# Performance work log

Measured on AMD Instinct MI355X. Metric: run time of the kernel, lower is better.

The kernel has to match this reference:

```python
import jax, jax.numpy as jnp
import numpy as np

NUM_HEADS = 16
EPS = 1e-5

def _lif(z, vth=1.0):
    # MyNode with fresh membrane and a single call: out = (0/tau + z >= vth)
    return (z >= vth).astype(z.dtype)

def _bn(z, g, b):
    # BatchNorm1d in train mode on (M, C, N): batch stats over (M, N)
    mu = z.mean(axis=(0, 2), keepdims=True)
    var = ((z - mu) ** 2).mean(axis=(0, 2), keepdims=True)
    return g[None, :, None] * (z - mu) * jax.lax.rsqrt(var + EPS) + b[None, :, None]

def _conv1(z, w, bias=None):
    # 1x1 Conv1d: (M, C, N) x (D, C) -> (M, D, N)
    out = jnp.einsum('mcn,dc->mdn', z, w)
    if bias is not None:
        out = out + bias[None, :, None]
    return out

def _rpb_matrix(P, N):
    # vectorized SCA_VA.compute_RPB_matrix: B[i*W+j, k*W+l] = P[(i-k)+M-1, (j-l)+M-1]
    Hs = int(round(N ** 0.5)); M = Hs + 1
    d = jnp.arange(Hs)[:, None] - jnp.arange(Hs)[None, :] + (M - 1)  # (Hs, Hs)
    Bm = P[d[:, None, :, None], d[None, :, None, :]]  # [i, j, k, l]
    return Bm.reshape(N, N)

def _sca(x, y, W, G, Bt, rpb=None):
    # shared body of SCA_AV / SCA_VA; W:(4,C,C) = [q,k,v,proj], G/Bt:(4,C) BN affine
    T, B, C, N = x.shape
    H = NUM_HEADS; D = C // H
    xf = x.reshape(T * B, C, N); yf = y.reshape(T * B, C, N)
    def branch(src, i):
        s = _lif(_bn(_conv1(src, W[i]), G[i], Bt[i]))  # (TB, C, N) binary spikes
        return s.reshape(T, B, C, N).transpose(0, 1, 3, 2).reshape(T, B, N, H, D).transpose(0, 1, 3, 2, 4)
    q = branch(xf, 0)  # (T,B,H,N,D)
    k = branch(yf, 1)
    v = branch(yf, 2)
    attn = jnp.einsum('tbhnd,tbhmd->tbhnm', q, k)  # no softmax: raw spike q@k^T
    if rpb is not None:
        attn = _lif(attn + rpb[None, None, None])  # rpb_lif (v_threshold=1.0)
    o = jnp.einsum('tbhnm,tbhmd->tbhnd', attn, v) * 0.25  # self.scale = 0.25
    o = o.transpose(0, 1, 2, 4, 3).reshape(T, B, C, N)
    o = _lif(o.reshape(T * B, C, N), 0.5)  # attn_lif v_threshold=0.5
    o = _lif(_bn(_conv1(o, W[3]), G[3], Bt[3]))  # proj_conv + proj_bn + proj_lif
    return o.reshape(T, B, C, N)

def _forward(x, y, av_w, av_g, av_b, va_w, va_g, va_b, P_rpb,
             fc1_w, fc1_b, fc2_w, fc2_b,
             m1_w, m1_b, m1_g, m1_bb, m2_w, m2_b, m2_g, m2_bb):
    T, B, C, N = x.shape
    # cross-modal spiking attention (visual->audio and audio->visual)
    x1 = x + _sca(x, y, av_w, av_g, av_b)                       # SCA_AV(x, y)
    y1 = y + _sca(y, x, va_w, va_g, va_b, rpb=_rpb_matrix(P_rpb, N))  # SCA_VA(y, x)
    # CMCI fusion: Linear on channel dim of transposed tensors, then LIF
    zx = jnp.einsum('tbcn,dc->tbdn', x1, fc1_w) + fc1_b[None, None, :, None]
    zy = jnp.einsum('tbcn,dc->tbdn', y1, fc2_w) + fc2_b[None, None, :, None]
    cur = _lif(zx + zy)  # (T,B,C,N)
    # MLPBlock: residual MLP (conv1x1 -> BN -> LIF) x 2
    cf = cur.reshape(T * B, C, N)
    h = _lif(_bn(_conv1(cf, m1_w, m1_b), m1_g, m1_bb))
    o = _lif(_bn(_conv1(h, m2_w, m2_b), m2_g, m2_bb))
    return cur + o.reshape(T, B, C, N)

def setup_inputs() -> dict:
    key = jax.random.key(0)
    ks = jax.random.split(key, 16)
    T, B, C, N = 4, 8, 256, 196
    Hd = 4 * C
    M2 = 2 * (int(N ** 0.5) + 1) - 1  # 29
    s = 0.05
    return {
        'x': jax.random.normal(ks[0], (T, B, C, N), jnp.float32),
        'y': jax.random.normal(ks[1], (T, B, C, N), jnp.float32),
        'av_w': jax.random.normal(ks[2], (4, C, C), jnp.float32) * s,
        'av_g': jnp.ones((4, C), jnp.float32),
        'av_b': jnp.zeros((4, C), jnp.float32),
        'va_w': jax.random.normal(ks[3], (4, C, C), jnp.float32) * s,
        'va_g': jnp.ones((4, C), jnp.float32),
        'va_b': jnp.zeros((4, C), jnp.float32),
        'P_rpb': jax.random.normal(ks[4], (M2, M2), jnp.float32),
        'fc1_w': jax.random.normal(ks[5], (C, C), jnp.float32) * s,
        'fc1_b': jnp.zeros((C,), jnp.float32),
        'fc2_w': jax.random.normal(ks[6], (C, C), jnp.float32) * s,
        'fc2_b': jnp.zeros((C,), jnp.float32),
        'm1_w': jax.random.normal(ks[7], (Hd, C), jnp.float32) * s,
        'm1_b': jnp.zeros((Hd,), jnp.float32),
        'm1_g': jnp.ones((Hd,), jnp.float32),
        'm1_bb': jnp.zeros((Hd,), jnp.float32),
        'm2_w': jax.random.normal(ks[8], (C, Hd), jnp.float32) * s,
        'm2_b': jnp.zeros((C,), jnp.float32),
        'm2_g': jnp.ones((C,), jnp.float32),
        'm2_bb': jnp.zeros((C,), jnp.float32),
    }

def reference(x, y, av_w, av_g, av_b, va_w, va_g, va_b, P_rpb,
              fc1_w, fc1_b, fc2_w, fc2_b,
              m1_w, m1_b, m1_g, m1_bb, m2_w, m2_b, m2_g, m2_bb):
    return _forward(x, y, av_w, av_g, av_b, va_w, va_g, va_b, P_rpb,
                    fc1_w, fc1_b, fc2_w, fc2_b,
                    m1_w, m1_b, m1_g, m1_bb, m2_w, m2_b, m2_g, m2_bb)
```

## Files before the change

### kernel.cpp

```cpp
#include <hip/hip_runtime.h>
#include <math.h>

#define TBB 32
#define CC  256
#define NN  196
#define NJ  (TBB * NN)
#define HD  1024
#define SLAB   ((size_t)TBB * CC * NN)
#define SLAB1K ((size_t)TBB * HD * NN)

struct Ptr6  { const float* p[6]; };
struct PtrM6 { float*       p[6]; };

struct GArg {
    const float* W;  const float* In;
    const float* W2; const float* In2;
    const float* bias; const float* bias2;
    float* Z;
};
struct GArgs { GArg a[6]; };

__device__ __forceinline__ void async_copy16(const float* gsrc, float* ldst)
{
    typedef __attribute__((address_space(1))) void GV;
    typedef __attribute__((address_space(3))) void LV;
    __builtin_amdgcn_global_load_lds((GV*)const_cast<float*>(gsrc), (LV*)ldst,
                                     16, 0, 0);
}

__global__ __launch_bounds__(256) void gemm2(GArgs ga, int Cout, int Cin, int mode)
{
    __shared__ __align__(16) float As[2][16][68];
    __shared__ __align__(16) float Bs[2][16][64];

    const GArg g = ga.a[blockIdx.z];
    const int t  = threadIdx.x;
    const int tx = t & 15, ty = t >> 4;
    const int d0 = blockIdx.x * 64;
    const int j0 = blockIdx.y * 64;
    const int lane = t & 63, wave = t >> 6;

    const int wrow = t >> 2;
    const int wk   = (t & 3) * 4;

    const int brow = wave * 4 + (lane >> 4);
    const int bj   = j0 + (lane & 15) * 4;
    const int bm   = bj / NN;
    const int bn   = bj - bm * NN;
    const size_t bbase = (size_t)bm * Cin * NN + bn;
    float* bdst0 = &Bs[0][wave * 4][0];
    float* bdst1 = &Bs[1][wave * 4][0];

    float acc[4][4] = {{0.f}};
    float4 wreg;

    for (int pass = 0; pass < 2; ++pass) {
        const float* Wp = pass ? g.W2 : g.W;
        const float* Ip = pass ? g.In2 : g.In;
        if (Wp == nullptr) break;
        const int nkt = Cin >> 4;
        const size_t wbase = (size_t)(d0 + wrow) * Cin + wk;

        async_copy16(Ip + bbase + (size_t)brow * NN, bdst0);
        wreg = *(const float4*)(Wp + wbase);
        As[0][wk + 0][wrow] = wreg.x;
        As[0][wk + 1][wrow] = wreg.y;
        As[0][wk + 2][wrow] = wreg.z;
        As[0][wk + 3][wrow] = wreg.w;
        __syncthreads();

        for (int kt = 0; kt < nkt; ++kt) {
            const int  cur  = kt & 1;
            const int  nxt  = cur ^ 1;
            const bool more = (kt + 1) < nkt;
            if (more) {
                const int k0n = (kt + 1) << 4;
                async_copy16(Ip + bbase + (size_t)(k0n + brow) * NN,
                             nxt ? bdst1 : bdst0);
                wreg = *(const float4*)(Wp + wbase + k0n);
            }
            #pragma unroll
            for (int kk = 0; kk < 16; ++kk) {
                const float4 a4 = *(const float4*)(&As[cur][kk][ty * 4]);
                const float4 b4 = *(const float4*)(&Bs[cur][kk][tx * 4]);
                const float ar[4] = {a4.x, a4.y, a4.z, a4.w};
                const float br[4] = {b4.x, b4.y, b4.z, b4.w};
                #pragma unroll
                for (int i = 0; i < 4; ++i)
                    #pragma unroll
                    for (int jj = 0; jj < 4; ++jj)
                        acc[i][jj] = fmaf(ar[i], br[jj], acc[i][jj]);
            }
            if (more) {
                As[nxt][wk + 0][wrow] = wreg.x;
                As[nxt][wk + 1][wrow] = wreg.y;
                As[nxt][wk + 2][wrow] = wreg.z;
                As[nxt][wk + 3][wrow] = wreg.w;
            }
            __syncthreads();
        }
    }

    #pragma unroll
    for (int i = 0; i < 4; ++i) {
        const int d = d0 + ty * 4 + i;
        float bv = 0.f;
        if (g.bias)  bv += g.bias[d];
        if (g.bias2) bv += g.bias2[d];
        #pragma unroll
        for (int jj = 0; jj < 4; ++jj) {
            const int j = j0 + tx * 4 + jj;
            const int m = j / NN;
            const int n = j - m * NN;
            const float v = acc[i][jj] + bv;
            g.Z[(size_t)(m * Cout + d) * NN + n] =
                (mode == 1) ? ((v >= 1.f) ? 1.f : 0.f) : v;
        }
    }
}

__global__ __launch_bounds__(256) void bn_stats(
    Ptr6 Zs, Ptr6 gs, Ptr6 bs, int Cout,
    float* __restrict__ scale, float* __restrict__ shift)
{
    const int d = blockIdx.x, g = blockIdx.y, t = threadIdx.x;
    const float* Z = Zs.p[g];
    double s = 0.0, s2 = 0.0;
    for (int i = t; i < NJ; i += 256) {
        int m = i / NN, n = i - m * NN;
        double v = (double)Z[(size_t)(m * Cout + d) * NN + n];
        s += v; s2 += v * v;
    }
    __shared__ double sh[256], sh2[256];
    sh[t] = s; sh2[t] = s2;
    __syncthreads();
    for (int off = 128; off > 0; off >>= 1) {
        if (t < off) { sh[t] += sh[t + off]; sh2[t] += sh2[t + off]; }
        __syncthreads();
    }
    if (t == 0) {
        double mu  = sh[0] / (double)NJ;
        double var = sh2[0] / (double)NJ - mu * mu;
        double a   = (double)gs.p[g][d] / sqrt(var + 1e-5);
        scale[g * Cout + d] = (float)a;
        shift[g * Cout + d] = (float)((double)bs.p[g][d] - mu * a);
    }
}

__global__ __launch_bounds__(256) void bn_apply2(
    Ptr6 Zs, PtrM6 Ss, Ptr6 Rs, const float* __restrict__ scale,
    const float* __restrict__ shift, int Cout, int total4, int mode)
{
    const int gix = blockIdx.y;
    const int i4  = blockIdx.x * 256 + threadIdx.x;
    if (i4 >= total4) return;
    const size_t base = (size_t)i4 * 4;
    const int d = (int)((base / NN) % (size_t)Cout);
    const float sc = scale[gix * Cout + d];
    const float sh = shift[gix * Cout + d];
    const float4 z = *(const float4*)(Zs.p[gix] + base);
    float4 o;
    o.x = (fmaf(sc, z.x, sh) >= 1.f) ? 1.f : 0.f;
    o.y = (fmaf(sc, z.y, sh) >= 1.f) ? 1.f : 0.f;
    o.z = (fmaf(sc, z.z, sh) >= 1.f) ? 1.f : 0.f;
    o.w = (fmaf(sc, z.w, sh) >= 1.f) ? 1.f : 0.f;
    if (mode == 1) {
        const float4 r = *(const float4*)(Rs.p[gix] + base);
        o.x += r.x; o.y += r.y; o.z += r.z; o.w += r.w;
    }
    *(float4*)(Ss.p[gix] + base) = o;
}

__global__ __launch_bounds__(256) void attention_k(
    const float* __restrict__ Q, const float* __restrict__ K,
    const float* __restrict__ V, const float* __restrict__ P,
    float* __restrict__ O)
{
    const int m = blockIdx.x;
    const int h = blockIdx.y;
    const int t = threadIdx.x;
    __shared__ unsigned int qb[196], kb[196], vb[196];
    __shared__ float Pl[841];

    if (P) { for (int i = t; i < 841; i += 256) Pl[i] = P[i]; }
    if (t < 196) {
        unsigned int q = 0, k = 0, v = 0;
        size_t base = (size_t)m * CC * NN + (size_t)h * 16 * NN + t;
        #pragma unroll
        for (int dd = 0; dd < 16; ++dd) {
            size_t off = base + (size_t)dd * NN;
            if (Q[off] > 0.5f) q |= (1u << dd);
            if (K[off] > 0.5f) k |= (1u << dd);
            if (V[off] > 0.5f) v |= (1u << dd);
        }
        qb[t] = q; kb[t] = k; vb[t] = v;
    }
    __syncthreads();

    if (t < 196) {
        int acc[16] = {0};
        const int ni = t / 14, nj = t - ni * 14;
        const unsigned int qr = qb[t];
        if (P) {
            for (int mm = 0; mm < 196; ++mm) {
                int a = __popc(qr & kb[mm]);
                int mi = mm / 14, mj = mm - mi * 14;
                float sv = (float)a + Pl[(ni - mi + 14) * 29 + (nj - mj + 14)];
                if (sv >= 1.f) {
                    unsigned int vv = vb[mm];
                    #pragma unroll
                    for (int dd = 0; dd < 16; ++dd)
                        acc[dd] += (vv >> dd) & 1;
                }
            }
        } else {
            for (int mm = 0; mm < 196; ++mm) {
                int a = __popc(qr & kb[mm]);
                if (a) {
                    unsigned int vv = vb[mm];
                    #pragma unroll
                    for (int dd = 0; dd < 16; ++dd)
                        acc[dd] += ((vv >> dd) & 1) ? a : 0;
                }
            }
        }
        size_t base = (size_t)m * CC * NN + (size_t)h * 16 * NN + t;
        #pragma unroll
        for (int dd = 0; dd < 16; ++dd)
            O[base + (size_t)dd * NN] = (acc[dd] >= 2) ? 1.f : 0.f;
    }
}

extern "C" void kernel_launch(void* const* d_in, const int* in_sizes, int n_in,
                              void* d_out, int out_size, void* d_ws, size_t ws_size,
                              hipStream_t stream)
{
    const float* x     = (const float*)d_in[0];
    const float* y     = (const float*)d_in[1];
    const float* av_w  = (const float*)d_in[2];
    const float* av_g  = (const float*)d_in[3];
    const float* av_b  = (const float*)d_in[4];
    const float* va_w  = (const float*)d_in[5];
    const float* va_g  = (const float*)d_in[6];
    const float* va_b  = (const float*)d_in[7];
    const float* P_rpb = (const float*)d_in[8];
    const float* fc1_w = (const float*)d_in[9];
    const float* fc1_b = (const float*)d_in[10];
    const float* fc2_w = (const float*)d_in[11];
    const float* fc2_b = (const float*)d_in[12];
    const float* m1_w  = (const float*)d_in[13];
    const float* m1_b  = (const float*)d_in[14];
    const float* m1_g  = (const float*)d_in[15];
    const float* m1_bb = (const float*)d_in[16];
    const float* m2_w  = (const float*)d_in[17];
    const float* m2_b  = (const float*)d_in[18];
    const float* m2_g  = (const float*)d_in[19];
    const float* m2_bb = (const float*)d_in[20];
    float* out = (float*)d_out;

    float* ws    = (float*)d_ws;
    float* A     = ws;
    float* Bf    = A  + 6 * SLAB;
    float* Cf    = Bf + 2 * SLAB;
    float* scale = Cf + 2 * SLAB;
    float* shift = scale + 6 * 1024;

    const size_t CC2 = (size_t)CC * CC;
    const int apply256  = (int)(SLAB / 4 / 256);
    const int apply1024 = (int)(SLAB1K / 4 / 256);

    GArgs ga{};
    {
        const float* Wl[6] = { av_w, av_w + CC2, av_w + 2*CC2, va_w, va_w + CC2, va_w + 2*CC2 };
        const float* Il[6] = { x, y, y, y, x, x };
        for (int i = 0; i < 6; ++i)
            ga.a[i] = GArg{ Wl[i], Il[i], nullptr, nullptr, nullptr, nullptr, A + i*SLAB };
    }
    gemm2<<<dim3(CC/64, NJ/64, 6), 256, 0, stream>>>(ga, CC, CC, 0);

    Ptr6 Zs{}, gs{}, bs{}, Rs{}; PtrM6 Ss{};
    {
        const float* gl[6] = { av_g, av_g + CC, av_g + 2*CC, va_g, va_g + CC, va_g + 2*CC };
        const float* bl[6] = { av_b, av_b + CC, av_b + 2*CC, va_b, va_b + CC, va_b + 2*CC };
        for (int i = 0; i < 6; ++i) {
            Zs.p[i] = A + i*SLAB; Ss.p[i] = A + i*SLAB; gs.p[i] = gl[i]; bs.p[i] = bl[i];
        }
    }
    bn_stats<<<dim3(CC, 6), 256, 0, stream>>>(Zs, gs, bs, CC, scale, shift);
    bn_apply2<<<dim3(apply256, 6), 256, 0, stream>>>(Zs, Ss, Rs, scale, shift, CC, (int)(SLAB/4), 0);

    attention_k<<<dim3(TBB, 16), 256, 0, stream>>>(A, A + SLAB, A + 2*SLAB, nullptr, Bf);
    attention_k<<<dim3(TBB, 16), 256, 0, stream>>>(A + 3*SLAB, A + 4*SLAB, A + 5*SLAB, P_rpb, Bf + SLAB);

    GArgs gc{};
    gc.a[0] = GArg{ av_w + 3*CC2, Bf,        nullptr, nullptr, nullptr, nullptr, Cf };
    gc.a[1] = GArg{ va_w + 3*CC2, Bf + SLAB, nullptr, nullptr, nullptr, nullptr, Cf + SLAB };
    gemm2<<<dim3(CC/64, NJ/64, 2), 256, 0, stream>>>(gc, CC, CC, 0);
    Zs.p[0] = Cf; Zs.p[1] = Cf + SLAB;
    gs.p[0] = av_g + 3*CC; gs.p[1] = va_g + 3*CC;
    bs.p[0] = av_b + 3*CC; bs.p[1] = va_b + 3*CC;
    Rs.p[0] = x; Rs.p[1] = y;
    Ss.p[0] = A; Ss.p[1] = A + SLAB;
    bn_stats<<<dim3(CC, 2), 256, 0, stream>>>(Zs, gs, bs, CC, scale, shift);
    bn_apply2<<<dim3(apply256, 2), 256, 0, stream>>>(Zs, Ss, Rs, scale, shift, CC, (int)(SLAB/4), 1);

    GArgs gf{};
    gf.a[0] = GArg{ fc1_w, A, fc2_w, A + SLAB, fc1_b, fc2_b, Bf + SLAB };
    gemm2<<<dim3(CC/64, NJ/64, 1), 256, 0, stream>>>(gf, CC, CC, 1);

    GArgs g1{};
    g1.a[0] = GArg{ m1_w, Bf + SLAB, nullptr, nullptr, m1_b, nullptr, A };
    gemm2<<<dim3(HD/64, NJ/64, 1), 256, 0, stream>>>(g1, HD, CC, 0);
    Zs.p[0] = A; Ss.p[0] = A; gs.p[0] = m1_g; bs.p[0] = m1_bb;
    bn_stats<<<dim3(HD, 1), 256, 0, stream>>>(Zs, gs, bs, HD, scale, shift);
    bn_apply2<<<dim3(apply1024, 1), 256, 0, stream>>>(Zs, Ss, Rs, scale, shift, HD, (int)(SLAB1K/4), 0);

    GArgs g2{};
    g2.a[0] = GArg{ m2_w, A, nullptr, nullptr, m2_b, nullptr, Cf };
    gemm2<<<dim3(CC/64, NJ/64, 1), 256, 0, stream>>>(g2, CC, HD, 0);
    Zs.p[0] = Cf; gs.p[0] = m2_g; bs.p[0] = m2_bb;
    Rs.p[0] = Bf + SLAB;
    Ss.p[0] = out;
    bn_stats<<<dim3(CC, 1), 256, 0, stream>>>(Zs, gs, bs, CC, scale, shift);
    bn_apply2<<<dim3(apply256, 1), 256, 0, stream>>>(Zs, Ss, Rs, scale, shift, CC, (int)(SLAB/4), 1);
}
```

Baseline: 541.5 us.

## Store binary spike tensors as uint8 and add byte-input GEMM kernel

Binary spike activations (q/k/v, attention output, fc output, MLP hidden) are now written as uint8 instead of float32, and a new gemm_u8 kernel reads byte-packed inputs with 32x128 tiles. The two attention launches are merged into one grid with a z dimension. This cuts memory traffic for spike tensors about fourfold and removes a launch. In exchange it adds byte-to-float conversion work inside the GEMM inner loop and uses narrow 4-byte async copies.

```diff
diff --git a/kernel.cpp b/kernel.cpp
--- a/kernel.cpp
+++ b/kernel.cpp
@@ -20,12 +20,24 @@
 };
 struct GArgs { GArg a[6]; };
 
+struct UArg {
+    const float* W; const unsigned char* In; const float* bias; float* Z;
+};
+struct UArgs { UArg a[2]; };
+
 __device__ __forceinline__ void async_copy16(const float* gsrc, float* ldst)
 {
     typedef __attribute__((address_space(1))) void GV;
     typedef __attribute__((address_space(3))) void LV;
     __builtin_amdgcn_global_load_lds((GV*)const_cast<float*>(gsrc), (LV*)ldst,
                                      16, 0, 0);
+}
+__device__ __forceinline__ void async_copy4(const unsigned char* gsrc, unsigned char* ldst)
+{
+    typedef __attribute__((address_space(1))) void GV;
+    typedef __attribute__((address_space(3))) void LV;
+    __builtin_amdgcn_global_load_lds((GV*)const_cast<unsigned char*>(gsrc), (LV*)ldst,
+                                     4, 0, 0);
 }
 
 __global__ __launch_bounds__(256) void gemm2(GArgs ga, int Cout, int Cin, int mode)
@@ -47,7 +59,6 @@
     const int bj   = j0 + (lane & 15) * 4;
     const int bm   = bj / NN;
     const int bn   = bj - bm * NN;
-    const size_t bbase = (size_t)bm * Cin * NN + bn;
     float* bdst0 = &Bs[0][wave * 4][0];
     float* bdst1 = &Bs[1][wave * 4][0];
 
@@ -60,6 +71,7 @@
         if (Wp == nullptr) break;
         const int nkt = Cin >> 4;
         const size_t wbase = (size_t)(d0 + wrow) * Cin + wk;
+        const size_t bbase = (size_t)bm * Cin * NN + bn;
 
         async_copy16(Ip + bbase + (size_t)brow * NN, bdst0);
         wreg = *(const float4*)(Wp + wbase);
@@ -81,10 +93,10 @@
             }
             #pragma unroll
             for (int kk = 0; kk < 16; ++kk) {
-                const float4 a4 = *(const float4*)(&As[cur][kk][ty * 4]);
-                const float4 b4 = *(const float4*)(&Bs[cur][kk][tx * 4]);
-                const float ar[4] = {a4.x, a4.y, a4.z, a4.w};
-                const float br[4] = {b4.x, b4.y, b4.z, b4.w};
+                float4 a4 = *(const float4*)(&As[cur][kk][ty * 4]);
+                float4 b4 = *(const float4*)(&Bs[cur][kk][tx * 4]);
+                float ar[4] = {a4.x, a4.y, a4.z, a4.w};
+                float br[4] = {b4.x, b4.y, b4.z, b4.w};
                 #pragma unroll
                 for (int i = 0; i < 4; ++i)
                     #pragma unroll
@@ -103,18 +115,123 @@
 
     #pragma unroll
     for (int i = 0; i < 4; ++i) {
-        const int d = d0 + ty * 4 + i;
+        int d = d0 + ty * 4 + i;
         float bv = 0.f;
         if (g.bias)  bv += g.bias[d];
         if (g.bias2) bv += g.bias2[d];
         #pragma unroll
         for (int jj = 0; jj < 4; ++jj) {
-            const int j = j0 + tx * 4 + jj;
+            int j = j0 + tx * 4 + jj;
+            int m = j / NN;
+            int n = j - m * NN;
+            float v = acc[i][jj] + bv;
+            if (mode == 2) {
+                ((unsigned char*)g.Z)[(size_t)(m * Cout + d) * NN + n] =
+                    (v >= 1.f) ? (unsigned char)1 : (unsigned char)0;
+            } else {
+                g.Z[(size_t)(m * Cout + d) * NN + n] =
+                    (mode == 1) ? ((v >= 1.f) ? 1.f : 0.f) : v;
+            }
+        }
+    }
+}
+
+__global__ __launch_bounds__(256) void gemm_u8(UArgs ua, int Cout, int Cin)
+{
+    __shared__ __align__(16) float         As[2][16][36];
+    __shared__ __align__(8)  unsigned char Bs[2][16][128];
+
+    const UArg g = ua.a[blockIdx.z];
+    const int t  = threadIdx.x;
+    const int tx = t & 15;
+    const int ty = t >> 4;
+    const int d0 = blockIdx.x * 32;
+    const int j0 = blockIdx.y * 128;
+    const int lane = t & 63, wave = t >> 6;
+
+    const int brow = 2 * wave + (lane >> 5);
+    const int bj   = j0 + (lane & 31) * 4;
+    const int bm   = bj / NN;
+    const int bn   = bj - bm * NN;
+    const size_t bbase = (size_t)bm * Cin * NN + bn;
+
+    const int wrow = (t & 127) >> 2;
+    const int wk   = (t & 3) * 4;
+    const size_t wbase = (size_t)(d0 + wrow) * Cin + wk;
+
+    float acc[2][8] = {{0.f}};
+    float4 wreg;
+    const int nkt = Cin >> 4;
+
+    async_copy4(g.In + bbase + (size_t)brow * NN,       &Bs[0][2 * wave][0]);
+    async_copy4(g.In + bbase + (size_t)(8 + brow) * NN, &Bs[0][8 + 2 * wave][0]);
+    if (t < 128) {
+        wreg = *(const float4*)(g.W + wbase);
+        As[0][wk + 0][wrow] = wreg.x;
+        As[0][wk + 1][wrow] = wreg.y;
+        As[0][wk + 2][wrow] = wreg.z;
+        As[0][wk + 3][wrow] = wreg.w;
+    }
+    __syncthreads();
+
+    for (int kt = 0; kt < nkt; ++kt) {
+        const int  cur  = kt & 1;
+        const int  nxt  = cur ^ 1;
+        const bool more = (kt + 1) < nkt;
+        if (more) {
+            const int k0n = (kt + 1) << 4;
+            async_copy4(g.In + bbase + (size_t)(k0n + brow) * NN,
+                        &Bs[nxt][2 * wave][0]);
+            async_copy4(g.In + bbase + (size_t)(k0n + 8 + brow) * NN,
+                        &Bs[nxt][8 + 2 * wave][0]);
+            if (t < 128) wreg = *(const float4*)(g.W + wbase + k0n);
+        }
+        #pragma unroll
+        for (int kk = 0; kk < 16; ++kk) {
+            const float2 a2 = *(const float2*)(&As[cur][kk][ty * 2]);
+            const uint2  bv = *(const uint2*)(&Bs[cur][kk][tx * 8]);
+            float br[8];
+            br[0] = (float)( bv.x        & 0xFF);
+            br[1] = (float)((bv.x >>  8) & 0xFF);
+            br[2] = (float)((bv.x >> 16) & 0xFF);
+            br[3] = (float)( bv.x >> 24        );
+            br[4] = (float)( bv.y        & 0xFF);
+            br[5] = (float)((bv.y >>  8) & 0xFF);
+            br[6] = (float)((bv.y >> 16) & 0xFF);
+            br[7] = (float)( bv.y >> 24        );
+            #pragma unroll
+            for (int i = 0; i < 2; ++i) {
+                const float a = i ? a2.y : a2.x;
+                #pragma unroll
+                for (int jj = 0; jj < 8; ++jj)
+                    acc[i][jj] = fmaf(a, br[jj], acc[i][jj]);
+            }
+        }
+        if (more && t < 128) {
+            As[nxt][wk + 0][wrow] = wreg.x;
+            As[nxt][wk + 1][wrow] = wreg.y;
+            As[nxt][wk + 2][wrow] = wreg.z;
+            As[nxt][wk + 3][wrow] = wreg.w;
+        }
+        __syncthreads();
+    }
+
+    const int jb = j0 + tx * 8;
+    #pragma unroll
+    for (int i = 0; i < 2; ++i) {
+        const int d = d0 + ty * 2 + i;
+        const float bv = g.bias ? g.bias[d] : 0.f;
+        #pragma unroll
+        for (int h = 0; h < 2; ++h) {
+            const int j = jb + h * 4;
             const int m = j / NN;
             const int n = j - m * NN;
-            const float v = acc[i][jj] + bv;
-            g.Z[(size_t)(m * Cout + d) * NN + n] =
-                (mode == 1) ? ((v >= 1.f) ? 1.f : 0.f) : v;
+            float4 o;
+            o.x = acc[i][h * 4 + 0] + bv;
+            o.y = acc[i][h * 4 + 1] + bv;
+            o.z = acc[i][h * 4 + 2] + bv;
+            o.w = acc[i][h * 4 + 3] + bv;
+            *(float4*)(g.Z + (size_t)(m * Cout + d) * NN + n) = o;
         }
     }
 }
@@ -165,23 +282,28 @@
     o.z = (fmaf(sc, z.z, sh) >= 1.f) ? 1.f : 0.f;
     o.w = (fmaf(sc, z.w, sh) >= 1.f) ? 1.f : 0.f;
     if (mode == 1) {
+        uchar4 u;
+        u.x = (unsigned char)o.x; u.y = (unsigned char)o.y;
+        u.z = (unsigned char)o.z; u.w = (unsigned char)o.w;
+        *(uchar4*)((unsigned char*)Ss.p[gix] + base) = u;
+        return;
+    }
+    if (mode == 2) {
         const float4 r = *(const float4*)(Rs.p[gix] + base);
         o.x += r.x; o.y += r.y; o.z += r.z; o.w += r.w;
+    } else if (mode == 3) {
+        const uchar4 r = *(const uchar4*)((const unsigned char*)Rs.p[gix] + base);
+        o.x += (float)r.x; o.y += (float)r.y; o.z += (float)r.z; o.w += (float)r.w;
     }
     *(float4*)(Ss.p[gix] + base) = o;
 }
 
-__global__ __launch_bounds__(256) void attention_k(
-    const float* __restrict__ Q, const float* __restrict__ K,
-    const float* __restrict__ V, const float* __restrict__ P,
-    float* __restrict__ O)
-{
-    const int m = blockIdx.x;
-    const int h = blockIdx.y;
-    const int t = threadIdx.x;
-    __shared__ unsigned int qb[196], kb[196], vb[196];
-    __shared__ float Pl[841];
-
+__device__ __forceinline__ void attention_body(
+    const unsigned char* __restrict__ Q, const unsigned char* __restrict__ K,
+    const unsigned char* __restrict__ V, const float* __restrict__ P,
+    unsigned char* __restrict__ O, int m, int h, int t,
+    unsigned int* qb, unsigned int* kb, unsigned int* vb, float* Pl)
+{
     if (P) { for (int i = t; i < 841; i += 256) Pl[i] = P[i]; }
     if (t < 196) {
         unsigned int q = 0, k = 0, v = 0;
@@ -189,9 +311,9 @@
         #pragma unroll
         for (int dd = 0; dd < 16; ++dd) {
             size_t off = base + (size_t)dd * NN;
-            if (Q[off] > 0.5f) q |= (1u << dd);
-            if (K[off] > 0.5f) k |= (1u << dd);
-            if (V[off] > 0.5f) v |= (1u << dd);
+            if (Q[off]) q |= (1u << dd);
+            if (K[off]) k |= (1u << dd);
+            if (V[off]) v |= (1u << dd);
         }
         qb[t] = q; kb[t] = k; vb[t] = v;
     }
@@ -227,8 +349,24 @@
         size_t base = (size_t)m * CC * NN + (size_t)h * 16 * NN + t;
         #pragma unroll
         for (int dd = 0; dd < 16; ++dd)
-            O[base + (size_t)dd * NN] = (acc[dd] >= 2) ? 1.f : 0.f;
-    }
+            O[base + (size_t)dd * NN] = (acc[dd] >= 2) ? 1 : 0;
+    }
+}
+
+__global__ __launch_bounds__(256) void attention_k2(
+    const unsigned char* __restrict__ Q0, const unsigned char* __restrict__ K0,
+    const unsigned char* __restrict__ V0, unsigned char* __restrict__ O0,
+    const unsigned char* __restrict__ Q1, const unsigned char* __restrict__ K1,
+    const unsigned char* __restrict__ V1, unsigned char* __restrict__ O1,
+    const float* __restrict__ P)
+{
+    __shared__ unsigned int qb[196], kb[196], vb[196];
+    __shared__ float Pl[841];
+    const int m = blockIdx.x, h = blockIdx.y, t = threadIdx.x;
+    if (blockIdx.z == 0)
+        attention_body(Q0, K0, V0, nullptr, O0, m, h, t, qb, kb, vb, Pl);
+    else
+        attention_body(Q1, K1, V1, P,       O1, m, h, t, qb, kb, vb, Pl);
 }
 
 extern "C" void kernel_launch(void* const* d_in, const int* in_sizes, int n_in,
@@ -265,6 +403,11 @@
     float* scale = Cf + 2 * SLAB;
     float* shift = scale + 6 * 1024;
 
+    unsigned char* Qu  = (unsigned char*)Bf;
+    unsigned char* Ou  = (unsigned char*)Cf;
+    unsigned char* cur = (unsigned char*)Bf;
+    unsigned char* Hu  = (unsigned char*)(Cf + SLAB);
+
     const size_t CC2 = (size_t)CC * CC;
     const int apply256  = (int)(SLAB / 4 / 256);
     const int apply1024 = (int)(SLAB1K / 4 / 256);
@@ -283,44 +426,53 @@
         const float* gl[6] = { av_g, av_g + CC, av_g + 2*CC, va_g, va_g + CC, va_g + 2*CC };
         const float* bl[6] = { av_b, av_b + CC, av_b + 2*CC, va_b, va_b + CC, va_b + 2*CC };
         for (int i = 0; i < 6; ++i) {
-            Zs.p[i] = A + i*SLAB; Ss.p[i] = A + i*SLAB; gs.p[i] = gl[i]; bs.p[i] = bl[i];
+            Zs.p[i] = A + i*SLAB;
+            Ss.p[i] = (float*)(Qu + i*SLAB);
+            gs.p[i] = gl[i]; bs.p[i] = bl[i];
         }
     }
     bn_stats<<<dim3(CC, 6), 256, 0, stream>>>(Zs, gs, bs, CC, scale, shift);
-    bn_apply2<<<dim3(apply256, 6), 256, 0, stream>>>(Zs, Ss, Rs, scale, shift, CC, (int)(SLAB/4), 0);
-
-    attention_k<<<dim3(TBB, 16), 256, 0, stream>>>(A, A + SLAB, A + 2*SLAB, nullptr, Bf);
-    attention_k<<<dim3(TBB, 16), 256, 0, stream>>>(A + 3*SLAB, A + 4*SLAB, A + 5*SLAB, P_rpb, Bf + SLAB);
-
-    GArgs gc{};
-    gc.a[0] = GArg{ av_w + 3*CC2, Bf,        nullptr, nullptr, nullptr, nullptr, Cf };
-    gc.a[1] = GArg{ va_w + 3*CC2, Bf + SLAB, nullptr, nullptr, nullptr, nullptr, Cf + SLAB };
-    gemm2<<<dim3(CC/64, NJ/64, 2), 256, 0, stream>>>(gc, CC, CC, 0);
-    Zs.p[0] = Cf; Zs.p[1] = Cf + SLAB;
+    bn_apply2<<<dim3(apply256, 6), 256, 0, stream>>>(Zs, Ss, Rs, scale, shift, CC, (int)(SLAB/4), 1);
+
+    attention_k2<<<dim3(TBB, 16, 2), 256, 0, stream>>>(
+        Qu, Qu + SLAB, Qu + 2*SLAB, Ou,
+        Qu + 3*SLAB, Qu + 4*SLAB, Qu + 5*SLAB, Ou + SLAB, P_rpb);
+
+    {
+        UArgs uc{};
+        uc.a[0] = UArg{ av_w + 3*CC2, Ou,        nullptr, A };
+        uc.a[1] = UArg{ va_w + 3*CC2, Ou + SLAB, nullptr, A + SLAB };
+        gemm_u8<<<dim3(CC/32, NJ/128, 2), 256, 0, stream>>>(uc, CC, CC);
+    }
+    Zs.p[0] = A; Zs.p[1] = A + SLAB;
     gs.p[0] = av_g + 3*CC; gs.p[1] = va_g + 3*CC;
     bs.p[0] = av_b + 3*CC; bs.p[1] = va_b + 3*CC;
     Rs.p[0] = x; Rs.p[1] = y;
-    Ss.p[0] = A; Ss.p[1] = A + SLAB;
+    Ss.p[0] = A + 2*SLAB; Ss.p[1] = A + 3*SLAB;
     bn_stats<<<dim3(CC, 2), 256, 0, stream>>>(Zs, gs, bs, CC, scale, shift);
-    bn_apply2<<<dim3(apply256, 2), 256, 0, stream>>>(Zs, Ss, Rs, scale, shift, CC, (int)(SLAB/4), 1);
+    bn_apply2<<<dim3(apply256, 2), 256, 0, stream>>>(Zs, Ss, Rs, scale, shift, CC, (int)(SLAB/4), 2);
 
     GArgs gf{};
-    gf.a[0] = GArg{ fc1_w, A, fc2_w, A + SLAB, fc1_b, fc2_b, Bf + SLAB };
-    gemm2<<<dim3(CC/64, NJ/64, 1), 256, 0, stream>>>(gf, CC, CC, 1);
-
-    GArgs g1{};
-    g1.a[0] = GArg{ m1_w, Bf + SLAB, nullptr, nullptr, m1_b, nullptr, A };
-    gemm2<<<dim3(HD/64, NJ/64, 1), 256, 0, stream>>>(g1, HD, CC, 0);
-    Zs.p[0] = A; Ss.p[0] = A; gs.p[0] = m1_g; bs.p[0] = m1_bb;
+    gf.a[0] = GArg{ fc1_w, A + 2*SLAB, fc2_w, A + 3*SLAB, fc1_b, fc2_b, (float*)cur };
+    gemm2<<<dim3(CC/64, NJ/64, 1), 256, 0, stream>>>(gf, CC, CC, 2);
+
+    {
+        UArgs u1{};
+        u1.a[0] = UArg{ m1_w, cur, m1_b, A };
+        gemm_u8<<<dim3(HD/32, NJ/128, 1), 256, 0, stream>>>(u1, HD, CC);
+    }
+    Zs.p[0] = A; Ss.p[0] = (float*)Hu; gs.p[0] = m1_g; bs.p[0] = m1_bb;
     bn_stats<<<dim3(HD, 1), 256, 0, stream>>>(Zs, gs, bs, HD, scale, shift);
-    bn_apply2<<<dim3(apply1024, 1), 256, 0, stream>>>(Zs, Ss, Rs, scale, shift, HD, (int)(SLAB1K/4), 0);
-
-    GArgs g2{};
-    g2.a[0] = GArg{ m2_w, A, nullptr, nullptr, m2_b, nullptr, Cf };
-    gemm2<<<dim3(CC/64, NJ/64, 1), 256, 0, stream>>>(g2, CC, HD, 0);
-    Zs.p[0] = Cf; gs.p[0] = m2_g; bs.p[0] = m2_bb;
-    Rs.p[0] = Bf + SLAB;
+    bn_apply2<<<dim3(apply1024, 1), 256, 0, stream>>>(Zs, Ss, Rs, scale, shift, HD, (int)(SLAB1K/4), 1);
+
+    {
+        UArgs u2{};
+        u2.a[0] = UArg{ m2_w, Hu, m2_b, Bf + SLAB };
+        gemm_u8<<<dim3(CC/32, NJ/128, 1), 256, 0, stream>>>(u2, CC, HD);
+    }
+    Zs.p[0] = Bf + SLAB; gs.p[0] = m2_g; bs.p[0] = m2_bb;
+    Rs.p[0] = (const float*)cur;
     Ss.p[0] = out;
     bn_stats<<<dim3(CC, 1), 256, 0, stream>>>(Zs, gs, bs, CC, scale, shift);
-    bn_apply2<<<dim3(apply256, 1), 256, 0, stream>>>(Zs, Ss, Rs, scale, shift, CC, (int)(SLAB/4), 1);
-}
+    bn_apply2<<<dim3(apply256, 1), 256, 0, stream>>>(Zs, Ss, Rs, scale, shift, CC, (int)(SLAB/4), 3);
+}
```

Result: slower. 554.0 us (+2.3%).
